# Performance work log

Measured on AMD Instinct MI355X. Metric: run time of the kernel, lower is better.

## Reference

```python
import jax, jax.numpy as jnp
import numpy as np

B, L, D_MODEL = 2, 1024, 512
N_LAYERS, D_STATE, D_CONV = 6, 16, 4
D_INNER = 2 * D_MODEL          # Mamba default expand=2
DT_RANK = (D_MODEL + 15) // 16  # ceil(d_model/16) = 32
EPS = 1.1920929e-07             # torch RMSNorm default eps (fp32 machine eps)


def rmsnorm(x, w):
    return x * jax.lax.rsqrt(jnp.mean(x * x, axis=-1, keepdims=True) + EPS) * w


def selective_scan(u, dt, A, Bm, Cm, Dv):
    # u, dt: (B,L,E); A: (E,N); Bm, Cm: (B,L,N); Dv: (E,)
    dA = jnp.exp(jnp.einsum('ble,en->blen', dt, A))    # discretized A (ZOH)
    dBu = jnp.einsum('ble,bln->blen', dt * u, Bm)      # discretized B * u (Euler)

    def step(h, inp):
        dA_t, dBu_t, C_t = inp
        h = dA_t * h + dBu_t                           # (B,E,N) state update
        y = jnp.einsum('ben,bn->be', h, C_t)
        return h, y

    h0 = jnp.zeros((u.shape[0], u.shape[2], A.shape[1]), u.dtype)
    _, ys = jax.lax.scan(step, h0,
                         (dA.transpose(1, 0, 2, 3), dBu.transpose(1, 0, 2, 3),
                          Cm.transpose(1, 0, 2)))
    return ys.transpose(1, 0, 2) + u * Dv


def mamba_block(x, p):
    xz = jnp.einsum('bld,ed->ble', x, p['in_proj_w'])  # (B,L,2E)
    xi, z = jnp.split(xz, 2, axis=-1)
    # causal depthwise conv1d (kernel D_CONV) + bias + SiLU
    xc = jnp.pad(xi.transpose(0, 2, 1), ((0, 0), (0, 0), (D_CONV - 1, 0)))
    xc = jax.lax.conv_general_dilated(xc, p['conv_w'][:, None, :], (1,), 'VALID',
                                      feature_group_count=D_INNER)
    xi = jax.nn.silu(xc.transpose(0, 2, 1) + p['conv_b'])
    dbc = jnp.einsum('ble,re->blr', xi, p['x_proj_w'])  # (B,L,R+2N)
    dt, Bm, Cm = jnp.split(dbc, [DT_RANK, DT_RANK + D_STATE], axis=-1)
    dt = jax.nn.softplus(jnp.einsum('blr,er->ble', dt, p['dt_w']) + p['dt_b'])
    y = selective_scan(xi, dt, -jnp.exp(p['A_log']), Bm, Cm, p['D'])
    y = y * jax.nn.silu(z)                              # gate branch
    return jnp.einsum('ble,de->bld', y, p['out_w'])


def setup_inputs() -> dict:
    key = jax.random.key(0)
    ks = jax.random.split(key, 8)
    s = 0.02
    return {
        'x': jax.random.normal(ks[0], (B, L, D_MODEL), jnp.float32),
        'position_embedding': jax.random.normal(ks[1], (B, L, D_MODEL), jnp.float32) * 0.02,
        'norm_w': jnp.ones((D_MODEL,), jnp.float32),
        'in_proj_w': jax.random.normal(ks[2], (N_LAYERS, 2 * D_INNER, D_MODEL), jnp.float32) * s,
        'conv_w': jax.random.normal(ks[3], (N_LAYERS, D_INNER, D_CONV), jnp.float32) * 0.2,
        'conv_b': jnp.zeros((N_LAYERS, D_INNER), jnp.float32),
        'x_proj_w': jax.random.normal(ks[4], (N_LAYERS, DT_RANK + 2 * D_STATE, D_INNER), jnp.float32) * s,
        'dt_w': jax.random.normal(ks[5], (N_LAYERS, D_INNER, DT_RANK), jnp.float32) * s,
        'dt_b': jnp.full((N_LAYERS, D_INNER), -4.6, jnp.float32),  # softplus(dt_b) ~ 0.01
        'A_log': jnp.broadcast_to(
            jnp.log(jnp.arange(1, D_STATE + 1, dtype=jnp.float32)),
            (N_LAYERS, D_INNER, D_STATE)) + jnp.zeros((N_LAYERS, D_INNER, D_STATE), jnp.float32),
        'D': jnp.ones((N_LAYERS, D_INNER), jnp.float32),
        'out_w': jax.random.normal(ks[6], (N_LAYERS, D_MODEL, D_INNER), jnp.float32) * s,
    }


def reference(x, position_embedding, norm_w, in_proj_w, conv_w, conv_b,
              x_proj_w, dt_w, dt_b, A_log, D, out_w):
    stacked = dict(in_proj_w=in_proj_w, conv_w=conv_w, conv_b=conv_b,
                   x_proj_w=x_proj_w, dt_w=dt_w, dt_b=dt_b,
                   A_log=A_log, D=D, out_w=out_w)

    def body(h, p):
        h = h + position_embedding          # added at the start of every layer
        h = mamba_block(rmsnorm(h, norm_w), p)  # NOTE: no residual, per source
        return h, None

    h, _ = jax.lax.scan(body, x, stacked)
    return h
```

## Files before the change

### kernel.cpp

```cpp
#include <hip/hip_runtime.h>
#include <hip/hip_bf16.h>


typedef __attribute__((ext_vector_type(8))) short bf16x8;
typedef __attribute__((ext_vector_type(4))) float f32x4;

__device__ __forceinline__ float bf2f(unsigned short u) {
    unsigned int x = ((unsigned int)u) << 16;
    return __builtin_bit_cast(float, x);
}
__device__ __forceinline__ unsigned short f2bf(float f) {
    __hip_bfloat16 h = __float2bfloat16(f);
    return __builtin_bit_cast(unsigned short, h);
}
__device__ __forceinline__ float ldin(const void* p, size_t i, int isbf) {
    return isbf ? bf2f(((const unsigned short*)p)[i]) : ((const float*)p)[i];
}
__device__ __forceinline__ float softplus_f(float x) {
    return (x > 20.f) ? x : log1pf(__expf(x));
}
__device__ __forceinline__ void split2(float x, unsigned short& h, unsigned short& l) {
    h = f2bf(x);
    l = f2bf(x - bf2f(h));
}

__global__ void dtype_probe(const void* __restrict__ D, int* __restrict__ flag) {
    *flag = (*(const unsigned int*)D == 0x3F800000u) ? 0 : 1;
}

__global__ __launch_bounds__(256) void cvt_in(const void* __restrict__ x,
                                              const int* __restrict__ flag,
                                              float* __restrict__ h, int n) {
    const int isbf = *flag;
    int g = blockIdx.x * 256 + threadIdx.x;
    if (g < n) h[g] = ldin(x, g, isbf);
}

__global__ __launch_bounds__(256) void wconv(const void* __restrict__ W,
                                             const int* __restrict__ flag,
                                             unsigned short* __restrict__ Wh,
                                             unsigned short* __restrict__ Wl, int n) {
    const int isbf = *flag;
    int g = blockIdx.x * 256 + threadIdx.x;
    if (g >= n) return;
    if (isbf) { Wh[g] = ((const unsigned short*)W)[g]; Wl[g] = 0; }
    else {
        unsigned short hh, ll;
        split2(((const float*)W)[g], hh, ll);
        Wh[g] = hh; Wl[g] = ll;
    }
}

template <int ACT>
__global__ __launch_bounds__(256) void gemm_hl(
    const unsigned short* __restrict__ Ah, const unsigned short* __restrict__ Al,
    int lda,
    const unsigned short* __restrict__ Wh, const unsigned short* __restrict__ Wl,
    long woff,
    float* __restrict__ Cf, long zstride,
    const void* __restrict__ bias, long boff, const int* __restrict__ flag,
    int N, int K, int Kc)
{
    const int isbf = *flag;
    __shared__ __align__(16) unsigned short As[2][64][40];
    __shared__ __align__(16) unsigned short Ws[2][64][40];

    const int m0 = blockIdx.x * 64, n0 = blockIdx.y * 64;
    const int kb = blockIdx.z * Kc;
    const int t = threadIdx.x;
    const int lane = t & 63, wave = t >> 6;
    const int wm = (wave & 1) * 32, wn = (wave >> 1) * 32;
    const int srow = t >> 2, scol = (t & 3) * 8;

    const unsigned short* ah = Ah + (size_t)(m0 + srow) * lda + scol;
    const unsigned short* al = Al + (size_t)(m0 + srow) * lda + scol;
    const unsigned short* wh = Wh + woff + (size_t)(n0 + srow) * K + scol;
    const unsigned short* wl = Wl + woff + (size_t)(n0 + srow) * K + scol;

    f32x4 acc[2][2] = {};

    for (int k0 = kb; k0 < kb + Kc; k0 += 32) {
        __syncthreads();
        *(uint4*)(&As[0][srow][scol]) = *(const uint4*)(ah + k0);
        *(uint4*)(&As[1][srow][scol]) = *(const uint4*)(al + k0);
        *(uint4*)(&Ws[0][srow][scol]) = *(const uint4*)(wh + k0);
        *(uint4*)(&Ws[1][srow][scol]) = *(const uint4*)(wl + k0);
        __syncthreads();

        const int fm = lane & 15, fk = (lane >> 4) * 8;
        bf16x8 a0h = *(const bf16x8*)(&As[0][wm + fm][fk]);
        bf16x8 a1h = *(const bf16x8*)(&As[0][wm + 16 + fm][fk]);
        bf16x8 w0h = *(const bf16x8*)(&Ws[0][wn + fm][fk]);
        bf16x8 w1h = *(const bf16x8*)(&Ws[0][wn + 16 + fm][fk]);
        bf16x8 a0l = *(const bf16x8*)(&As[1][wm + fm][fk]);
        bf16x8 a1l = *(const bf16x8*)(&As[1][wm + 16 + fm][fk]);
        bf16x8 w0l = *(const bf16x8*)(&Ws[1][wn + fm][fk]);
        bf16x8 w1l = *(const bf16x8*)(&Ws[1][wn + 16 + fm][fk]);

        acc[0][0] = __builtin_amdgcn_mfma_f32_16x16x32_bf16(a0h, w0h, acc[0][0], 0, 0, 0);
        acc[0][1] = __builtin_amdgcn_mfma_f32_16x16x32_bf16(a0h, w1h, acc[0][1], 0, 0, 0);
        acc[1][0] = __builtin_amdgcn_mfma_f32_16x16x32_bf16(a1h, w0h, acc[1][0], 0, 0, 0);
        acc[1][1] = __builtin_amdgcn_mfma_f32_16x16x32_bf16(a1h, w1h, acc[1][1], 0, 0, 0);
        acc[0][0] = __builtin_amdgcn_mfma_f32_16x16x32_bf16(a0h, w0l, acc[0][0], 0, 0, 0);
        acc[0][1] = __builtin_amdgcn_mfma_f32_16x16x32_bf16(a0h, w1l, acc[0][1], 0, 0, 0);
        acc[1][0] = __builtin_amdgcn_mfma_f32_16x16x32_bf16(a1h, w0l, acc[1][0], 0, 0, 0);
        acc[1][1] = __builtin_amdgcn_mfma_f32_16x16x32_bf16(a1h, w1l, acc[1][1], 0, 0, 0);
        acc[0][0] = __builtin_amdgcn_mfma_f32_16x16x32_bf16(a0l, w0h, acc[0][0], 0, 0, 0);
        acc[0][1] = __builtin_amdgcn_mfma_f32_16x16x32_bf16(a0l, w1h, acc[0][1], 0, 0, 0);
        acc[1][0] = __builtin_amdgcn_mfma_f32_16x16x32_bf16(a1l, w0h, acc[1][0], 0, 0, 0);
        acc[1][1] = __builtin_amdgcn_mfma_f32_16x16x32_bf16(a1l, w1h, acc[1][1], 0, 0, 0);
    }

    float* Cp = Cf + (size_t)blockIdx.z * zstride;
    const int col = lane & 15, rb = (lane >> 4) * 4;
#pragma unroll
    for (int mi = 0; mi < 2; ++mi)
#pragma unroll
        for (int ni = 0; ni < 2; ++ni)
#pragma unroll
            for (int r = 0; r < 4; ++r) {
                int gm = m0 + wm + mi * 16 + rb + r;
                int gn = n0 + wn + ni * 16 + col;
                float v = acc[mi][ni][r];
                if (bias) v += ldin(bias, boff + gn, isbf);
                if (ACT == 1) v = softplus_f(v);
                Cp[(size_t)gm * N + gn] = v;
            }
}

__global__ __launch_bounds__(256) void xp_reduce(
    const float* __restrict__ Pxp, float* __restrict__ dbc,
    unsigned short* __restrict__ dth, unsigned short* __restrict__ dtl)
{
    int g = blockIdx.x * 256 + threadIdx.x;
    float s = 0.f;
#pragma unroll
    for (int z = 0; z < 8; ++z) s += Pxp[(size_t)z * 131072 + g];
    dbc[g] = s;
    int n = g & 63, t = g >> 6;
    if (n < 32) {
        unsigned short hh, ll;
        split2(s, hh, ll);
        dth[t * 32 + n] = hh; dtl[t * 32 + n] = ll;
    }
}

__global__ __launch_bounds__(256) void rmsnorm_k(
    const float* __restrict__ h, const void* __restrict__ pos,
    const void* __restrict__ nw, const int* __restrict__ flag,
    unsigned short* __restrict__ xnh, unsigned short* __restrict__ xnl)
{
    const int isbf = *flag;
    const int row = blockIdx.x;
    const int t = threadIdx.x;
    const size_t base = (size_t)row * 512;
    float v0 = h[base + t]       + ldin(pos, base + t, isbf);
    float v1 = h[base + 256 + t] + ldin(pos, base + 256 + t, isbf);
    float ss = v0 * v0 + v1 * v1;
#pragma unroll
    for (int o = 32; o; o >>= 1) ss += __shfl_xor(ss, o, 64);
    __shared__ float sw[4];
    if ((t & 63) == 0) sw[t >> 6] = ss;
    __syncthreads();
    float tot = sw[0] + sw[1] + sw[2] + sw[3];
    float sc = rsqrtf(tot * (1.0f / 512.0f) + 1.1920929e-07f);
    float o0 = v0 * sc * ldin(nw, t, isbf);
    float o1 = v1 * sc * ldin(nw, 256 + t, isbf);
    unsigned short hh, ll;
    split2(o0, hh, ll); xnh[base + t] = hh;       xnl[base + t] = ll;
    split2(o1, hh, ll); xnh[base + 256 + t] = hh; xnl[base + 256 + t] = ll;
}

__global__ __launch_bounds__(256) void conv_silu_k(
    const float* __restrict__ xz,
    const void* __restrict__ cw, long cwoff,
    const void* __restrict__ cb, long cboff,
    const int* __restrict__ flag,
    float* __restrict__ xi,
    unsigned short* __restrict__ xih, unsigned short* __restrict__ xil)
{
    const int isbf = *flag;
    int g = blockIdx.x * 256 + threadIdx.x;
    int e = g & 1023;
    int l = (g >> 10) & 1023;
    int b = g >> 20;
    float acc = ldin(cb, cboff + e, isbf);
#pragma unroll
    for (int k = 0; k < 4; ++k) {
        int ls = l - 3 + k;
        if (ls >= 0)
            acc += ldin(cw, cwoff + e * 4 + k, isbf) *
                   xz[((size_t)(b * 1024 + ls)) * 2048 + e];
    }
    acc = acc / (1.f + __expf(-acc));
    xi[g] = acc;
    unsigned short hh, ll;
    split2(acc, hh, ll);
    xih[g] = hh; xil[g] = ll;
}


#define CL 16
#define NCH 64

__global__ __launch_bounds__(256) void scan_stage1(
    const float* __restrict__ dtp, const float* __restrict__ u,
    const float* __restrict__ dbc,
    const void* __restrict__ alog, long aoff, const int* __restrict__ flag,
    float* __restrict__ P, float* __restrict__ S)
{
    const int isbf = *flag;
    int g = blockIdx.x * 256 + threadIdx.x;
    int e = g & 1023, c = (g >> 10) & (NCH - 1), b = g >> 16;
    int t0 = b * 1024 + c * CL;

    float dv[CL], uv[CL];
#pragma unroll
    for (int i = 0; i < CL; ++i) {
        dv[i] = dtp[(size_t)(t0 + i) * 1024 + e];
        uv[i] = u[(size_t)(t0 + i) * 1024 + e];
    }

    float Aen[16], Pn[16], Sn[16];
#pragma unroll
    for (int n = 0; n < 16; ++n) {
        Aen[n] = -__expf(ldin(alog, aoff + e * 16 + n, isbf));
        Pn[n] = 1.f; Sn[n] = 0.f;
    }
#pragma unroll
    for (int i = 0; i < CL; ++i) {
        float d = dv[i], du = d * uv[i];
        const float4* Bp = (const float4*)(dbc + (size_t)(t0 + i) * 64 + 32);
        float4 b0 = Bp[0], b1 = Bp[1], b2 = Bp[2], b3 = Bp[3];
        float Bt[16] = {b0.x,b0.y,b0.z,b0.w, b1.x,b1.y,b1.z,b1.w,
                        b2.x,b2.y,b2.z,b2.w, b3.x,b3.y,b3.z,b3.w};
#pragma unroll
        for (int n = 0; n < 16; ++n) {
            float a = __expf(d * Aen[n]);
            Sn[n] = a * Sn[n] + du * Bt[n];
            Pn[n] *= a;
        }
    }
    size_t ob = ((size_t)(b * NCH + c) * 16) * 1024 + e;
#pragma unroll
    for (int n = 0; n < 16; ++n) {
        P[ob + (size_t)n * 1024] = Pn[n];
        S[ob + (size_t)n * 1024] = Sn[n];
    }
}

__global__ __launch_bounds__(256) void scan_stage2(
    float* __restrict__ PH, const float* __restrict__ S)
{
    int g = blockIdx.x * 256 + threadIdx.x;
    int e = g & 1023, n = (g >> 10) & 15, b = g >> 14;
    float H = 0.f;
#pragma unroll 4
    for (int c = 0; c < NCH; ++c) {
        size_t idx = ((size_t)(b * NCH + c) * 16 + n) * 1024 + e;
        float p = PH[idx], s = S[idx];
        PH[idx] = H;
        H = p * H + s;
    }
}

__global__ __launch_bounds__(256) void scan_stage3(
    const float* __restrict__ dtp, const float* __restrict__ u,
    const float* __restrict__ dbc,
    const void* __restrict__ alog, long aoff,
    const void* __restrict__ Dv, long doff,
    const int* __restrict__ flag,
    const float* __restrict__ xz, const float* __restrict__ H0,
    unsigned short* __restrict__ yh, unsigned short* __restrict__ yl)
{
    const int isbf = *flag;
    int g = blockIdx.x * 256 + threadIdx.x;
    int e = g & 1023, c = (g >> 10) & (NCH - 1), b = g >> 16;
    int t0 = b * 1024 + c * CL;

    float dv[CL], uv[CL], zv[CL];
#pragma unroll
    for (int i = 0; i < CL; ++i) {
        dv[i] = dtp[(size_t)(t0 + i) * 1024 + e];
        uv[i] = u[(size_t)(t0 + i) * 1024 + e];
        zv[i] = xz[(size_t)(t0 + i) * 2048 + 1024 + e];
    }

    float Aen[16], h[16];
    size_t ob = ((size_t)(b * NCH + c) * 16) * 1024 + e;
#pragma unroll
    for (int n = 0; n < 16; ++n) {
        Aen[n] = -__expf(ldin(alog, aoff + e * 16 + n, isbf));
        h[n] = H0[ob + (size_t)n * 1024];
    }
    float De = ldin(Dv, doff + e, isbf);
#pragma unroll
    for (int i = 0; i < CL; ++i) {
        float d = dv[i], uu = uv[i], du = d * uu;
        const float4* Bp = (const float4*)(dbc + (size_t)(t0 + i) * 64 + 32);
        float4 b0 = Bp[0], b1 = Bp[1], b2 = Bp[2], b3 = Bp[3];
        float4 c0 = Bp[4], c1 = Bp[5], c2 = Bp[6], c3 = Bp[7];
        float Bt[16] = {b0.x,b0.y,b0.z,b0.w, b1.x,b1.y,b1.z,b1.w,
                        b2.x,b2.y,b2.z,b2.w, b3.x,b3.y,b3.z,b3.w};
        float Ct[16] = {c0.x,c0.y,c0.z,c0.w, c1.x,c1.y,c1.z,c1.w,
                        c2.x,c2.y,c2.z,c2.w, c3.x,c3.y,c3.z,c3.w};
        float y = 0.f;
#pragma unroll
        for (int n = 0; n < 16; ++n) {
            float a = __expf(d * Aen[n]);
            h[n] = a * h[n] + du * Bt[n];
            y += h[n] * Ct[n];
        }
        float sz = zv[i] / (1.f + __expf(-zv[i]));
        float yv = (y + uu * De) * sz;
        unsigned short hh, ll;
        split2(yv, hh, ll);
        yh[(size_t)(t0 + i) * 1024 + e] = hh;
        yl[(size_t)(t0 + i) * 1024 + e] = ll;
    }
}

extern "C" void kernel_launch(void* const* d_in, const int* in_sizes, int n_in,
                              void* d_out, int out_size, void* d_ws, size_t ws_size,
                              hipStream_t stream)
{
    const void* x    = d_in[0];
    const void* pos  = d_in[1];
    const void* nw   = d_in[2];
    const void* ipw  = d_in[3];
    const void* cw   = d_in[4];
    const void* cb   = d_in[5];
    const void* xpw  = d_in[6];
    const void* dtw  = d_in[7];
    const void* dtb  = d_in[8];
    const void* alog = d_in[9];
    const void* Dw   = d_in[10];
    const void* ow   = d_in[11];

    char* w = (char*)d_ws;
    auto take = [&](size_t bytes) { char* p = w; w += (bytes + 255) & ~255ull; return p; };

    float* h    = (float*)take(2048ull * 512 * 4);
    float* xz   = (float*)take(2048ull * 2048 * 4);
    float* xi   = (float*)take(2048ull * 1024 * 4);
    float* dtf  = (float*)take(2048ull * 1024 * 4);
    float* dbc  = (float*)take(2048ull * 64 * 4);
    float* P    = (float*)take(2ull * NCH * 16 * 1024 * 4);
    float* S    = (float*)take(2ull * NCH * 16 * 1024 * 4);
    float* Pxp  = (float*)take(8ull * 2048 * 64 * 4);
    unsigned short* xnh = (unsigned short*)take(2048ull * 512 * 2);
    unsigned short* xnl = (unsigned short*)take(2048ull * 512 * 2);
    unsigned short* xih = (unsigned short*)take(2048ull * 1024 * 2);
    unsigned short* xil = (unsigned short*)take(2048ull * 1024 * 2);
    unsigned short* yh  = (unsigned short*)take(2048ull * 1024 * 2);
    unsigned short* yl  = (unsigned short*)take(2048ull * 1024 * 2);
    unsigned short* dth = (unsigned short*)take(2048ull * 32 * 2);
    unsigned short* dtl = (unsigned short*)take(2048ull * 32 * 2);
    unsigned short* wip_h = (unsigned short*)take(6ull * 2048 * 512 * 2);
    unsigned short* wip_l = (unsigned short*)take(6ull * 2048 * 512 * 2);
    unsigned short* wow_h = (unsigned short*)take(6ull * 512 * 1024 * 2);
    unsigned short* wow_l = (unsigned short*)take(6ull * 512 * 1024 * 2);
    unsigned short* wxp_h = (unsigned short*)take(6ull * 64 * 1024 * 2);
    unsigned short* wxp_l = (unsigned short*)take(6ull * 64 * 1024 * 2);
    unsigned short* wdt_h = (unsigned short*)take(6ull * 1024 * 32 * 2);
    unsigned short* wdt_l = (unsigned short*)take(6ull * 1024 * 32 * 2);
    int* flag = (int*)take(256);

    dtype_probe<<<1, 1, 0, stream>>>(Dw, flag);
    cvt_in<<<4096, 256, 0, stream>>>(x, flag, h, 2048 * 512);
    wconv<<<24576, 256, 0, stream>>>(ipw, flag, wip_h, wip_l, 6 * 2048 * 512);
    wconv<<<12288, 256, 0, stream>>>(ow,  flag, wow_h, wow_l, 6 * 512 * 1024);
    wconv<<<1536, 256, 0, stream>>>(xpw, flag, wxp_h, wxp_l, 6 * 64 * 1024);
    wconv<<<768,  256, 0, stream>>>(dtw, flag, wdt_h, wdt_l, 6 * 1024 * 32);

    for (int l = 0; l < 6; ++l) {
        rmsnorm_k<<<2048, 256, 0, stream>>>(h, pos, nw, flag, xnh, xnl);
        gemm_hl<0><<<dim3(32, 32), 256, 0, stream>>>(
            xnh, xnl, 512, wip_h, wip_l, (long)l * 2048 * 512,
            xz, 0, nullptr, 0, flag, 2048, 512, 512);
        conv_silu_k<<<8192, 256, 0, stream>>>(xz, cw, (long)l * 4096, cb, (long)l * 1024,
                                              flag, xi, xih, xil);
        gemm_hl<0><<<dim3(32, 1, 8), 256, 0, stream>>>(
            xih, xil, 1024, wxp_h, wxp_l, (long)l * 64 * 1024,
            Pxp, 2048l * 64, nullptr, 0, flag, 64, 1024, 128);
        xp_reduce<<<512, 256, 0, stream>>>(Pxp, dbc, dth, dtl);
        gemm_hl<1><<<dim3(32, 16), 256, 0, stream>>>(
            dth, dtl, 32, wdt_h, wdt_l, (long)l * 1024 * 32,
            dtf, 0, dtb, (long)l * 1024, flag, 1024, 32, 32);
        scan_stage1<<<512, 256, 0, stream>>>(dtf, xi, dbc, alog, (long)l * 16384,
                                             flag, P, S);
        scan_stage2<<<128, 256, 0, stream>>>(P, S);
        scan_stage3<<<512, 256, 0, stream>>>(dtf, xi, dbc, alog, (long)l * 16384,
                                             Dw, (long)l * 1024, flag, xz, P, yh, yl);
        float* outp = (l < 5) ? h : (float*)d_out;
        gemm_hl<0><<<dim3(32, 8), 256, 0, stream>>>(
            yh, yl, 1024, wow_h, wow_l, (long)l * 512 * 1024,
            outp, 0, nullptr, 0, flag, 512, 1024, 1024);
    }
}
```

Baseline: 877.8 us.

## Add 128x128 MFMA GEMM for in_proj, fuse weight prep kernels, batch scan loads

Adds a 128x128-tile split-bf16 MFMA GEMM for the in_proj projection, replacing the 64x64 generic kernel so each block reuses more data per tile. The dtype probe, input conversion and four weight-split kernels are merged into one launch, and layer 0's RMSNorm now reads the raw input directly. The stage-2 scan now loads eight chunks before its dependent recurrence to expose more memory parallelism. Larger tiles give only 256 blocks and raise register and LDS use, which may lower occupancy.

After: 860.1 us. 2.0% less time.

```diff
diff --git a/kernel.cpp b/kernel.cpp
--- a/kernel.cpp
+++ b/kernel.cpp
@@ -24,31 +24,101 @@
     l = f2bf(x - bf2f(h));
 }
 
-__global__ void dtype_probe(const void* __restrict__ D, int* __restrict__ flag) {
-    *flag = (*(const unsigned int*)D == 0x3F800000u) ? 0 : 1;
-}
-
-__global__ __launch_bounds__(256) void cvt_in(const void* __restrict__ x,
-                                              const int* __restrict__ flag,
-                                              float* __restrict__ h, int n) {
-    const int isbf = *flag;
-    int g = blockIdx.x * 256 + threadIdx.x;
-    if (g < n) h[g] = ldin(x, g, isbf);
-}
-
-__global__ __launch_bounds__(256) void wconv(const void* __restrict__ W,
-                                             const int* __restrict__ flag,
-                                             unsigned short* __restrict__ Wh,
-                                             unsigned short* __restrict__ Wl, int n) {
-    const int isbf = *flag;
-    int g = blockIdx.x * 256 + threadIdx.x;
-    if (g >= n) return;
-    if (isbf) { Wh[g] = ((const unsigned short*)W)[g]; Wl[g] = 0; }
-    else {
-        unsigned short hh, ll;
-        split2(((const float*)W)[g], hh, ll);
-        Wh[g] = hh; Wl[g] = ll;
-    }
+#define S1 (6*2048*512)
+#define S2 (6*512*1024)
+#define S3 (6*64*1024)
+#define S4 (6*1024*32)
+__global__ __launch_bounds__(256) void wsplit_all(
+    const void* __restrict__ ipw, const void* __restrict__ ow,
+    const void* __restrict__ xpw, const void* __restrict__ dtw,
+    const void* __restrict__ Dw,
+    unsigned short* __restrict__ h1, unsigned short* __restrict__ l1,
+    unsigned short* __restrict__ h2, unsigned short* __restrict__ l2,
+    unsigned short* __restrict__ h3, unsigned short* __restrict__ l3,
+    unsigned short* __restrict__ h4, unsigned short* __restrict__ l4,
+    int* __restrict__ flag)
+{
+    int g = blockIdx.x * 256 + threadIdx.x;
+    const int isbf = (*(const unsigned int*)Dw == 0x3F800000u) ? 0 : 1;
+    if (g == 0) *flag = isbf;
+    const void* src; unsigned short *dh, *dl; int i;
+    if (g < S1)                { src = ipw; dh = h1; dl = l1; i = g; }
+    else if (g < S1+S2)        { src = ow;  dh = h2; dl = l2; i = g - S1; }
+    else if (g < S1+S2+S3)     { src = xpw; dh = h3; dl = l3; i = g - S1 - S2; }
+    else if (g < S1+S2+S3+S4)  { src = dtw; dh = h4; dl = l4; i = g - S1 - S2 - S3; }
+    else return;
+    unsigned short hh, ll;
+    split2(ldin(src, i, isbf), hh, ll);
+    dh[i] = hh; dl[i] = ll;
+}
+
+__global__ __launch_bounds__(256) void gemm128(
+    const unsigned short* __restrict__ Ah, const unsigned short* __restrict__ Al,
+    int lda,
+    const unsigned short* __restrict__ Wh, const unsigned short* __restrict__ Wl,
+    long woff,
+    float* __restrict__ Cf, int N, int K)
+{
+    __shared__ __align__(16) unsigned short As[2][128][40];
+    __shared__ __align__(16) unsigned short Ws[2][128][40];
+
+    const int m0 = blockIdx.x * 128, n0 = blockIdx.y * 128;
+    const int t = threadIdx.x, lane = t & 63, wave = t >> 6;
+    const int wm = (wave & 1) * 64, wn = (wave >> 1) * 64;
+    const int srow = t >> 1, scol = (t & 1) * 16;
+
+    const unsigned short* ah = Ah + (size_t)(m0 + srow) * lda + scol;
+    const unsigned short* al = Al + (size_t)(m0 + srow) * lda + scol;
+    const unsigned short* wh = Wh + woff + (size_t)(n0 + srow) * K + scol;
+    const unsigned short* wl = Wl + woff + (size_t)(n0 + srow) * K + scol;
+
+    f32x4 acc[4][4] = {};
+    const int fm = lane & 15, fk = (lane >> 4) * 8;
+
+    for (int k0 = 0; k0 < K; k0 += 32) {
+        __syncthreads();
+        *(uint4*)(&As[0][srow][scol])     = *(const uint4*)(ah + k0);
+        *(uint4*)(&As[0][srow][scol + 8]) = *(const uint4*)(ah + k0 + 8);
+        *(uint4*)(&As[1][srow][scol])     = *(const uint4*)(al + k0);
+        *(uint4*)(&As[1][srow][scol + 8]) = *(const uint4*)(al + k0 + 8);
+        *(uint4*)(&Ws[0][srow][scol])     = *(const uint4*)(wh + k0);
+        *(uint4*)(&Ws[0][srow][scol + 8]) = *(const uint4*)(wh + k0 + 8);
+        *(uint4*)(&Ws[1][srow][scol])     = *(const uint4*)(wl + k0);
+        *(uint4*)(&Ws[1][srow][scol + 8]) = *(const uint4*)(wl + k0 + 8);
+        __syncthreads();
+
+        bf16x8 a_h[4], a_l[4], w_h[4], w_l[4];
+#pragma unroll
+        for (int i = 0; i < 4; ++i) {
+            a_h[i] = *(const bf16x8*)(&As[0][wm + i * 16 + fm][fk]);
+            a_l[i] = *(const bf16x8*)(&As[1][wm + i * 16 + fm][fk]);
+            w_h[i] = *(const bf16x8*)(&Ws[0][wn + i * 16 + fm][fk]);
+            w_l[i] = *(const bf16x8*)(&Ws[1][wn + i * 16 + fm][fk]);
+        }
+#pragma unroll
+        for (int mi = 0; mi < 4; ++mi)
+#pragma unroll
+            for (int ni = 0; ni < 4; ++ni) {
+                acc[mi][ni] = __builtin_amdgcn_mfma_f32_16x16x32_bf16(
+                    a_h[mi], w_h[ni], acc[mi][ni], 0, 0, 0);
+                acc[mi][ni] = __builtin_amdgcn_mfma_f32_16x16x32_bf16(
+                    a_h[mi], w_l[ni], acc[mi][ni], 0, 0, 0);
+                acc[mi][ni] = __builtin_amdgcn_mfma_f32_16x16x32_bf16(
+                    a_l[mi], w_h[ni], acc[mi][ni], 0, 0, 0);
+            }
+    }
+
+    const int col = lane & 15, rb = (lane >> 4) * 4;
+#pragma unroll
+    for (int mi = 0; mi < 4; ++mi)
+#pragma unroll
+        for (int ni = 0; ni < 4; ++ni)
+#pragma unroll
+            for (int r = 0; r < 4; ++r) {
+                int gm = m0 + wm + mi * 16 + rb + r;
+                int gn = n0 + wn + ni * 16 + col;
+                Cf[(size_t)gm * N + gn] = acc[mi][ni][r];
+            }
 }
 
 template <int ACT>
@@ -146,7 +216,7 @@
 }
 
 __global__ __launch_bounds__(256) void rmsnorm_k(
-    const float* __restrict__ h, const void* __restrict__ pos,
+    const void* __restrict__ hsrc, int hdyn, const void* __restrict__ pos,
     const void* __restrict__ nw, const int* __restrict__ flag,
     unsigned short* __restrict__ xnh, unsigned short* __restrict__ xnl)
 {
@@ -154,8 +224,10 @@
     const int row = blockIdx.x;
     const int t = threadIdx.x;
     const size_t base = (size_t)row * 512;
-    float v0 = h[base + t]       + ldin(pos, base + t, isbf);
-    float v1 = h[base + 256 + t] + ldin(pos, base + 256 + t, isbf);
+    float h0 = hdyn ? ldin(hsrc, base + t, isbf)       : ((const float*)hsrc)[base + t];
+    float h1 = hdyn ? ldin(hsrc, base + 256 + t, isbf) : ((const float*)hsrc)[base + 256 + t];
+    float v0 = h0 + ldin(pos, base + t, isbf);
+    float v1 = h1 + ldin(pos, base + 256 + t, isbf);
     float ss = v0 * v0 + v1 * v1;
 #pragma unroll
     for (int o = 32; o; o >>= 1) ss += __shfl_xor(ss, o, 64);
@@ -199,7 +271,6 @@
     xih[g] = hh; xil[g] = ll;
 }
 
-
 #define CL 16
 #define NCH 64
 
@@ -255,12 +326,19 @@
     int g = blockIdx.x * 256 + threadIdx.x;
     int e = g & 1023, n = (g >> 10) & 15, b = g >> 14;
     float H = 0.f;
-#pragma unroll 4
-    for (int c = 0; c < NCH; ++c) {
-        size_t idx = ((size_t)(b * NCH + c) * 16 + n) * 1024 + e;
-        float p = PH[idx], s = S[idx];
-        PH[idx] = H;
-        H = p * H + s;
+    for (int cb = 0; cb < NCH; cb += 8) {
+        float p[8], s[8];
+#pragma unroll
+        for (int j = 0; j < 8; ++j) {
+            size_t idx = ((size_t)(b * NCH + cb + j) * 16 + n) * 1024 + e;
+            p[j] = PH[idx]; s[j] = S[idx];
+        }
+#pragma unroll
+        for (int j = 0; j < 8; ++j) {
+            size_t idx = ((size_t)(b * NCH + cb + j) * 16 + n) * 1024 + e;
+            PH[idx] = H;
+            H = p[j] * H + s[j];
+        }
     }
 }
 
@@ -366,18 +444,15 @@
     unsigned short* wdt_l = (unsigned short*)take(6ull * 1024 * 32 * 2);
     int* flag = (int*)take(256);
 
-    dtype_probe<<<1, 1, 0, stream>>>(Dw, flag);
-    cvt_in<<<4096, 256, 0, stream>>>(x, flag, h, 2048 * 512);
-    wconv<<<24576, 256, 0, stream>>>(ipw, flag, wip_h, wip_l, 6 * 2048 * 512);
-    wconv<<<12288, 256, 0, stream>>>(ow,  flag, wow_h, wow_l, 6 * 512 * 1024);
-    wconv<<<1536, 256, 0, stream>>>(xpw, flag, wxp_h, wxp_l, 6 * 64 * 1024);
-    wconv<<<768,  256, 0, stream>>>(dtw, flag, wdt_h, wdt_l, 6 * 1024 * 32);
+    wsplit_all<<<(S1 + S2 + S3 + S4 + 255) / 256, 256, 0, stream>>>(
+        ipw, ow, xpw, dtw, Dw,
+        wip_h, wip_l, wow_h, wow_l, wxp_h, wxp_l, wdt_h, wdt_l, flag);
 
     for (int l = 0; l < 6; ++l) {
-        rmsnorm_k<<<2048, 256, 0, stream>>>(h, pos, nw, flag, xnh, xnl);
-        gemm_hl<0><<<dim3(32, 32), 256, 0, stream>>>(
-            xnh, xnl, 512, wip_h, wip_l, (long)l * 2048 * 512,
-            xz, 0, nullptr, 0, flag, 2048, 512, 512);
+        rmsnorm_k<<<2048, 256, 0, stream>>>(
+            l == 0 ? x : (const void*)h, l == 0 ? 1 : 0, pos, nw, flag, xnh, xnl);
+        gemm128<<<dim3(16, 16), 256, 0, stream>>>(
+            xnh, xnl, 512, wip_h, wip_l, (long)l * 2048 * 512, xz, 2048, 512);
         conv_silu_k<<<8192, 256, 0, stream>>>(xz, cw, (long)l * 4096, cb, (long)l * 1024,
                                               flag, xi, xih, xil);
         gemm_hl<0><<<dim3(32, 1, 8), 256, 0, stream>>>(
```
